# Optimization experiments

Measured on AMD Instinct MI355X. Metric: run time of the kernel, lower is better.

The kernel has to match this reference:

```python
import jax, jax.numpy as jnp
import numpy as np

NEG = 16          # negative_samples
SKIP = 1          # skip_step


def setup_inputs() -> dict:
    key = jax.random.key(0)
    k1, k2, k3, k4 = jax.random.split(key, 4)
    B, C, H, Wd = 16, 256, 32, 32
    K = 5
    maxN = (H - SKIP - 1) * Wd * B          # largest y'*x*B (k=1)
    z = jax.random.normal(k1, (B, C, H, Wd), dtype=jnp.float32)
    c = jax.random.normal(k2, (B, C, H, Wd), dtype=jnp.float32)
    # 1x1 conv weights W_k: [K, out, in]; scaled so scores are O(1)
    W = jax.random.normal(k3, (K, C, C), dtype=jnp.float32) * (1.0 / C)
    rand_index = jax.random.randint(k4, (K, maxN * NEG), 0, maxN, dtype=jnp.int32)
    return {"z": z, "c": c, "W": W, "rand_index": rand_index}


def reference(z, c, W, rand_index):
    # CLAPP/CPC hinge contrastive loss, contrast_mode='hinge', gating=None,
    # which_update='both', no_gamma=False.
    K = W.shape[0]
    total_loss = jnp.float32(0.0)
    for k in range(1, K + 1):
        # ztwk = W_k(z[:, :, k+skip:, :]) permuted to [y, x, B, C]
        zt = z[:, :, k + SKIP:, :]                              # [B, C, y, x]
        ztwk = jnp.einsum('bcyx,oc->yxbo', zt, W[k - 1])        # [y, x, B, O]
        y, x, b, o = ztwk.shape
        N = y * x * b
        # negative sampling: gather NEG random rows of flattened ztwk
        flat = ztwk.reshape(N, o)
        idx = rand_index[k - 1, :N * NEG] % N                   # in-range indices
        ztwk_shuf = flat[idx].reshape(y, x, b, NEG, o)          # [y, x, B, neg, C]
        # context = c[:, :, :-(k+skip), :] permuted to [y, x, B, C]
        ctx = jnp.transpose(c[:, :, :-(k + SKIP), :], (2, 3, 0, 1))
        scores_pos = jnp.einsum('yxbc,yxbc->yxb', ctx, ztwk)            # [y, x, B]
        scores_neg = jnp.einsum('yxbc,yxbnc->yxbn', ctx, ztwk_shuf)     # [y, x, B, neg]
        # CLAPPHingeLoss (no_gamma=False): clamped hinge terms
        losses_pos = jnp.where(scores_pos < 1.0, 1.0 - scores_pos, 0.0)
        losses_neg = jnp.where(scores_neg > -1.0, 1.0 + scores_neg, 0.0)
        # per-sample means over (neg, y, x) then mean over batch; pos is
        # replicated over neg in the original, which leaves the mean unchanged
        loss_k = losses_pos.mean(axis=(0, 1)).mean() + losses_neg.mean(axis=(0, 1, 3)).mean()
        total_loss = total_loss + loss_k
    return total_loss
```

## Files before the change

kernel.cpp:

```cpp
#include <hip/hip_runtime.h>


typedef unsigned short u16;
typedef unsigned char u8;
typedef unsigned int u32;
typedef __attribute__((ext_vector_type(8))) short bf16x8;
typedef __attribute__((ext_vector_type(4))) float f32x4;
typedef __attribute__((ext_vector_type(2))) float f32x2;

#define NEG_  16
#define MAXN_ 15360
#define TOTROWS 71680
#define NSCORE 17920
#define NPOSP  1120
#define NPARTS (NSCORE + NPOSP)

__device__ __forceinline__ u16 f2bf(float f) {
    union { u32 i; float f; } v; v.f = f;
    u32 b = v.i;
    return (u16)((b + 0x7FFFu + ((b >> 16) & 1u)) >> 16);
}

__device__ __forceinline__ size_t frag_addr(int row, int k) {
    return ((size_t)(row >> 4) * 8 + (k >> 5)) * 512
         + (size_t)((row & 15) + 16 * ((k >> 3) & 3)) * 8 + (k & 7);
}

__global__ __launch_bounds__(256) void transpose_kernel(
    const float* __restrict__ z, const float* __restrict__ cc,
    const float* __restrict__ W,
    u16* __restrict__ ztr, u8* __restrict__ ct8, u16* __restrict__ Wbf)
{
    int tid = threadIdx.x;
    if (blockIdx.z == 2) {
        if (blockIdx.y != 0 || blockIdx.x >= 320) return;
        int i4 = blockIdx.x * 256 + tid;
        float4 v = reinterpret_cast<const float4*>(W)[i4];
        int e = i4 * 4;
        int kw = e >> 16;
        int rem = e & 65535;
        int o = rem >> 8, c = rem & 255;
        size_t base = (size_t)kw * 65536 + frag_addr(o, c);
        ushort4 u;
        u.x = f2bf(v.x); u.y = f2bf(v.y); u.z = f2bf(v.z); u.w = f2bf(v.w);
        *reinterpret_cast<ushort4*>(Wbf + base) = u;
        return;
    }
    int by = blockIdx.x;
    int b = by >> 5, y = by & 31;
    int c0 = blockIdx.y * 64;
    bool is_c = (blockIdx.z == 1);
    if (is_c && y >= 30) return;
    const float* src = is_c ? cc : z;

    __shared__ float ts[64][33];
    int x = tid & 31, ci0 = tid >> 5;
#pragma unroll
    for (int i = 0; i < 8; ++i) {
        int ci = ci0 + i * 8;
        ts[ci][x] = src[(((size_t)b * 256 + c0 + ci) * 32 + y) * 32 + x];
    }
    __syncthreads();
    int cw = tid & 63, xw0 = tid >> 6;
    if (is_c) {
#pragma unroll
        for (int i = 0; i < 8; ++i) {
            int xw = xw0 + i * 4;
            float v = ts[cw][xw];
            u32 pk = __builtin_amdgcn_cvt_pk_fp8_f32(v, v, 0, false);
            ct8[(((size_t)y * 32 + xw) * 16 + b) * 256 + c0 + cw] = (u8)pk;
        }
    } else {
        int k = c0 + cw;
#pragma unroll
        for (int i = 0; i < 8; ++i) {
            int xw = xw0 + i * 4;
            int row = (y * 32 + xw) * 16 + b;
            ztr[frag_addr(row, k)] = f2bf(ts[cw][xw]);
        }
    }
}

__global__ __launch_bounds__(256) void gemm_mfma_kernel(
    const u16* __restrict__ ztr, const u16* __restrict__ Wbf,
    const u8* __restrict__ ct8,
    u8* __restrict__ ztwk8, float* __restrict__ posPart)
{
    int flat = blockIdx.x;
    int kidx, base;
    if (flat < 240)      { kidx = 0; base = 0; }
    else if (flat < 472) { kidx = 1; base = 240; }
    else if (flat < 696) { kidx = 2; base = 472; }
    else if (flat < 912) { kidx = 3; base = 696; }
    else                 { kidx = 4; base = 912; }
    int row0 = (flat - base) * 64;
    int offk = 512 * (30 * kidx - (kidx * (kidx - 1)) / 2);

    int tile0 = (((kidx + 2) * 512 + row0) >> 4);
    const u16* Bsw = Wbf + (size_t)kidx * 65536;
    u8* out = ztwk8 + ((size_t)offk + row0) * 256;

    int wid = threadIdx.x >> 6, lane = threadIdx.x & 63;
    int col0 = wid * 64;

    const u16* Abase = ztr + (size_t)tile0 * 8 * 512 + lane * 8;
    const u16* Bbase = Bsw + (size_t)wid * 4 * 8 * 512 + lane * 8;

    f32x4 acc[4][4] = {};
    bf16x8 a[4], b[4];

#pragma unroll
    for (int i = 0; i < 4; ++i)
        a[i] = *reinterpret_cast<const bf16x8*>(Abase + (size_t)i * 8 * 512);
#pragma unroll
    for (int j = 0; j < 4; ++j)
        b[j] = *reinterpret_cast<const bf16x8*>(Bbase + (size_t)j * 8 * 512);

#pragma unroll
    for (int kb = 0; kb < 8; ++kb) {
        bf16x8 a2[4], b2[4];
        if (kb < 7) {
#pragma unroll
            for (int i = 0; i < 4; ++i)
                a2[i] = *reinterpret_cast<const bf16x8*>(Abase + ((size_t)i * 8 + kb + 1) * 512);
#pragma unroll
            for (int j = 0; j < 4; ++j)
                b2[j] = *reinterpret_cast<const bf16x8*>(Bbase + ((size_t)j * 8 + kb + 1) * 512);
        }
#pragma unroll
        for (int i = 0; i < 4; ++i)
#pragma unroll
            for (int j = 0; j < 4; ++j)
                acc[i][j] = __builtin_amdgcn_mfma_f32_16x16x32_bf16(b[j], a[i], acc[i][j], 0, 0, 0);
        if (kb < 7) {
#pragma unroll
            for (int i = 0; i < 4; ++i) a[i] = a2[i];
#pragma unroll
            for (int j = 0; j < 4; ++j) b[j] = b2[j];
        }
    }

    int lr = lane & 15;
    int rq = (lane >> 4) * 4;
    __shared__ float pos[4][64];

#pragma unroll
    for (int i = 0; i < 4; ++i) {
        int local = row0 + i * 16 + lr;
        float pp = 0.f;
#pragma unroll
        for (int j = 0; j < 4; ++j) {
            u32 u = 0;
            u = __builtin_amdgcn_cvt_pk_fp8_f32(acc[i][j][0], acc[i][j][1], u, false);
            u = __builtin_amdgcn_cvt_pk_fp8_f32(acc[i][j][2], acc[i][j][3], u, true);
            *reinterpret_cast<u32*>(out + (size_t)(i * 16 + lr) * 256 + col0 + j * 16 + rq) = u;
            u32 cw_ = *reinterpret_cast<const u32*>(ct8 + (size_t)local * 256 + col0 + j * 16 + rq);
            f32x2 clo = __builtin_amdgcn_cvt_pk_f32_fp8(cw_, false);
            f32x2 chi = __builtin_amdgcn_cvt_pk_f32_fp8(cw_, true);
            pp = fmaf(acc[i][j][0], clo.x, pp);
            pp = fmaf(acc[i][j][1], clo.y, pp);
            pp = fmaf(acc[i][j][2], chi.x, pp);
            pp = fmaf(acc[i][j][3], chi.y, pp);
        }
        pp += __shfl_xor(pp, 16);
        pp += __shfl_xor(pp, 32);
        if (lane < 16) pos[wid][i * 16 + lane] = pp;
    }
    __syncthreads();

    if (threadIdx.x < 64) {
        float p = pos[0][threadIdx.x] + pos[1][threadIdx.x]
                + pos[2][threadIdx.x] + pos[3][threadIdx.x];
        float Nk = (float)((30 - kidx) * 512);
        float h = fmaxf(0.f, 1.f - p) / Nk;
#pragma unroll
        for (int s = 1; s < 64; s <<= 1) h += __shfl_xor(h, s);
        if (threadIdx.x == 0) posPart[flat] = h;
    }
}

__device__ __forceinline__ float dot16(uint4 nb, const f32x2* cp) {
    f32x2 d0 = {0.f, 0.f}, d1 = {0.f, 0.f};
    d0 += __builtin_amdgcn_cvt_pk_f32_fp8(nb.x, false) * cp[0];
    d1 += __builtin_amdgcn_cvt_pk_f32_fp8(nb.x, true)  * cp[1];
    d0 += __builtin_amdgcn_cvt_pk_f32_fp8(nb.y, false) * cp[2];
    d1 += __builtin_amdgcn_cvt_pk_f32_fp8(nb.y, true)  * cp[3];
    d0 += __builtin_amdgcn_cvt_pk_f32_fp8(nb.z, false) * cp[4];
    d1 += __builtin_amdgcn_cvt_pk_f32_fp8(nb.z, true)  * cp[5];
    d0 += __builtin_amdgcn_cvt_pk_f32_fp8(nb.w, false) * cp[6];
    d1 += __builtin_amdgcn_cvt_pk_f32_fp8(nb.w, true)  * cp[7];
    f32x2 d = d0 + d1;
    return d.x + d.y;
}

__global__ __launch_bounds__(256) void score_kernel(
    const u8* __restrict__ ztwk8, const u8* __restrict__ ct8,
    const int* __restrict__ rind, float* __restrict__ partials)
{
    __shared__ float red[4];
    int bid = blockIdx.x;
    int swb = (bid & 7) * 2240 + (bid >> 3);
    int wid = threadIdx.x >> 6, lane = threadIdx.x & 63;
    int gp = swb * 4 + wid;

    const int ends0 = 15360, ends1 = 30208, ends2 = 44544, ends3 = 58368;
    int kidx, off;
    if (gp < ends0)      { kidx = 0; off = 0; }
    else if (gp < ends1) { kidx = 1; off = ends0; }
    else if (gp < ends2) { kidx = 2; off = ends1; }
    else if (gp < ends3) { kidx = 3; off = ends2; }
    else                 { kidx = 4; off = ends3; }
    int Nk = (30 - kidx) * 512;
    int local = gp - off;

    int r = lane >> 4, c16 = lane & 15;

    const int* rbase = rind + (size_t)kidx * (MAXN_ * NEG_) + (size_t)local * NEG_ + r;
    int rv0 = rbase[0], rv1 = rbase[4], rv2 = rbase[8], rv3 = rbase[12];
    int i0 = rv0 >= Nk ? rv0 - Nk : rv0;
    int i1 = rv1 >= Nk ? rv1 - Nk : rv1;
    int i2 = rv2 >= Nk ? rv2 - Nk : rv2;
    int i3 = rv3 >= Nk ? rv3 - Nk : rv3;

    const u8* zb = ztwk8 + (size_t)off * 256 + c16 * 16;
    uint4 nb0 = *reinterpret_cast<const uint4*>(zb + (size_t)i0 * 256);
    uint4 nb1 = *reinterpret_cast<const uint4*>(zb + (size_t)i1 * 256);
    uint4 nb2 = *reinterpret_cast<const uint4*>(zb + (size_t)i2 * 256);
    uint4 nb3 = *reinterpret_cast<const uint4*>(zb + (size_t)i3 * 256);

    uint4 cw4 = *reinterpret_cast<const uint4*>(ct8 + (size_t)local * 256 + c16 * 16);
    f32x2 cp[8];
    cp[0] = __builtin_amdgcn_cvt_pk_f32_fp8(cw4.x, false);
    cp[1] = __builtin_amdgcn_cvt_pk_f32_fp8(cw4.x, true);
    cp[2] = __builtin_amdgcn_cvt_pk_f32_fp8(cw4.y, false);
    cp[3] = __builtin_amdgcn_cvt_pk_f32_fp8(cw4.y, true);
    cp[4] = __builtin_amdgcn_cvt_pk_f32_fp8(cw4.z, false);
    cp[5] = __builtin_amdgcn_cvt_pk_f32_fp8(cw4.z, true);
    cp[6] = __builtin_amdgcn_cvt_pk_f32_fp8(cw4.w, false);
    cp[7] = __builtin_amdgcn_cvt_pk_f32_fp8(cw4.w, true);

    float d0 = dot16(nb0, cp);
    float d1 = dot16(nb1, cp);
    float d2 = dot16(nb2, cp);
    float d3 = dot16(nb3, cp);

    d0 += __shfl_xor(d0, 1); d1 += __shfl_xor(d1, 1);
    d2 += __shfl_xor(d2, 1); d3 += __shfl_xor(d3, 1);
    d0 += __shfl_xor(d0, 2); d1 += __shfl_xor(d1, 2);
    d2 += __shfl_xor(d2, 2); d3 += __shfl_xor(d3, 2);
    d0 += __shfl_xor(d0, 4); d1 += __shfl_xor(d1, 4);
    d2 += __shfl_xor(d2, 4); d3 += __shfl_xor(d3, 4);
    d0 += __shfl_xor(d0, 8); d1 += __shfl_xor(d1, 8);
    d2 += __shfl_xor(d2, 8); d3 += __shfl_xor(d3, 8);

    float h = fmaxf(0.f, 1.f + d0) + fmaxf(0.f, 1.f + d1)
            + fmaxf(0.f, 1.f + d2) + fmaxf(0.f, 1.f + d3);

    float val = h * (1.0f / 16.0f);
    val += __shfl_xor(val, 16);
    val += __shfl_xor(val, 32);
    val *= 1.0f / (float)Nk;

    if (lane == 0) red[wid] = val;
    __syncthreads();
    if (threadIdx.x == 0)
        partials[bid] = red[0] + red[1] + red[2] + red[3];
}

__global__ __launch_bounds__(1024) void reduce_kernel(
    const float* __restrict__ comb, float* __restrict__ out)
{
    __shared__ float s[16];
    float a = 0.f;
    for (int i = threadIdx.x; i < NPARTS; i += 1024) a += comb[i];
#pragma unroll
    for (int t = 1; t < 64; t <<= 1) a += __shfl_xor(a, t);
    int w = threadIdx.x >> 6, lane = threadIdx.x & 63;
    if (lane == 0) s[w] = a;
    __syncthreads();
    if (threadIdx.x < 16) {
        float v = s[threadIdx.x];
#pragma unroll
        for (int t = 1; t < 16; t <<= 1) v += __shfl_xor(v, t);
        if (threadIdx.x == 0) out[0] = v;
    }
}

extern "C" void kernel_launch(void* const* d_in, const int* in_sizes, int n_in,
                              void* d_out, int out_size, void* d_ws, size_t ws_size,
                              hipStream_t stream) {
    const float* z    = (const float*)d_in[0];
    const float* c    = (const float*)d_in[1];
    const float* W    = (const float*)d_in[2];
    const int*   rind = (const int*)d_in[3];

    char* ws = (char*)d_ws;
    u16*   ztr     = (u16*)  (ws + 0);
    u8*    ct8     = (u8*)   (ws + 8388608);
    u8*    ztwk8   = (u8*)   (ws + 12320768);
    float* parts   = (float*)(ws + 30670848);
    float* posPart = (float*)(ws + 30742528);
    u16*   Wbf     = (u16*)  (ws + 30747008);
    float* out     = (float*)d_out;

    transpose_kernel<<<dim3(512, 4, 3), 256, 0, stream>>>(z, c, W, ztr, ct8, Wbf);
    gemm_mfma_kernel<<<dim3(NPOSP), 256, 0, stream>>>(ztr, Wbf, ct8, ztwk8, posPart);
    score_kernel<<<dim3(NSCORE), 256, 0, stream>>>(ztwk8, ct8, rind, parts);
    reduce_kernel<<<dim3(1), 1024, 0, stream>>>(parts, out);
}
```

Measured before the change: 72.29 us.

## Make score kernel persistent-style with ten rows per wave, simplify GEMM loads

The score kernel now launches 896 blocks of 512 threads, and each wave loops over 10 consecutive score rows, accumulating into one partial per wave. This removes the shared-memory block reduction and cuts the partial count. Random indices are now loaded as one int4 per lane instead of four strided scalar loads. The transpose also skips z rows y<2, which the GEMM never reads, and the GEMM drops its manual register double-buffering in favour of a plain per-kb load loop. The risks are lost latency hiding in the GEMM and fewer waves in flight for the gather-bound score phase.

New measurement: 75.76 us. +4.8%, slower.

```diff
diff --git a/kernel.cpp b/kernel.cpp
--- a/kernel.cpp
+++ b/kernel.cpp
@@ -11,9 +11,9 @@
 #define NEG_  16
 #define MAXN_ 15360
 #define TOTROWS 71680
-#define NSCORE 17920
+#define SWAVES 7168
 #define NPOSP  1120
-#define NPARTS (NSCORE + NPOSP)
+#define NPARTS (SWAVES + NPOSP)
 
 __device__ __forceinline__ u16 f2bf(float f) {
     union { u32 i; float f; } v; v.f = f;
@@ -50,7 +50,7 @@
     int b = by >> 5, y = by & 31;
     int c0 = blockIdx.y * 64;
     bool is_c = (blockIdx.z == 1);
-    if (is_c && y >= 30) return;
+    if (is_c ? (y >= 30) : (y < 2)) return;
     const float* src = is_c ? cc : z;
 
     __shared__ float ts[64][33];
@@ -103,41 +103,23 @@
     int wid = threadIdx.x >> 6, lane = threadIdx.x & 63;
     int col0 = wid * 64;
 
-    const u16* Abase = ztr + (size_t)tile0 * 8 * 512 + lane * 8;
-    const u16* Bbase = Bsw + (size_t)wid * 4 * 8 * 512 + lane * 8;
-
     f32x4 acc[4][4] = {};
-    bf16x8 a[4], b[4];
-
-#pragma unroll
-    for (int i = 0; i < 4; ++i)
-        a[i] = *reinterpret_cast<const bf16x8*>(Abase + (size_t)i * 8 * 512);
-#pragma unroll
-    for (int j = 0; j < 4; ++j)
-        b[j] = *reinterpret_cast<const bf16x8*>(Bbase + (size_t)j * 8 * 512);
-
-#pragma unroll
+
     for (int kb = 0; kb < 8; ++kb) {
-        bf16x8 a2[4], b2[4];
-        if (kb < 7) {
-#pragma unroll
-            for (int i = 0; i < 4; ++i)
-                a2[i] = *reinterpret_cast<const bf16x8*>(Abase + ((size_t)i * 8 + kb + 1) * 512);
-#pragma unroll
-            for (int j = 0; j < 4; ++j)
-                b2[j] = *reinterpret_cast<const bf16x8*>(Bbase + ((size_t)j * 8 + kb + 1) * 512);
-        }
+        bf16x8 a[4], b[4];
+#pragma unroll
+        for (int i = 0; i < 4; ++i)
+            a[i] = *reinterpret_cast<const bf16x8*>(
+                ztr + ((size_t)(tile0 + i) * 8 + kb) * 512 + lane * 8);
+#pragma unroll
+        for (int j = 0; j < 4; ++j)
+            b[j] = *reinterpret_cast<const bf16x8*>(
+                Bsw + ((size_t)(wid * 4 + j) * 8 + kb) * 512 + lane * 8);
 #pragma unroll
         for (int i = 0; i < 4; ++i)
 #pragma unroll
             for (int j = 0; j < 4; ++j)
                 acc[i][j] = __builtin_amdgcn_mfma_f32_16x16x32_bf16(b[j], a[i], acc[i][j], 0, 0, 0);
-        if (kb < 7) {
-#pragma unroll
-            for (int i = 0; i < 4; ++i) a[i] = a2[i];
-#pragma unroll
-            for (int j = 0; j < 4; ++j) b[j] = b2[j];
-        }
     }
 
     int lr = lane & 15;
@@ -193,78 +175,78 @@
     return d.x + d.y;
 }
 
-__global__ __launch_bounds__(256) void score_kernel(
+__global__ __launch_bounds__(512) void score_kernel(
     const u8* __restrict__ ztwk8, const u8* __restrict__ ct8,
     const int* __restrict__ rind, float* __restrict__ partials)
 {
-    __shared__ float red[4];
     int bid = blockIdx.x;
-    int swb = (bid & 7) * 2240 + (bid >> 3);
+    int swb = (bid & 7) * 112 + (bid >> 3);
     int wid = threadIdx.x >> 6, lane = threadIdx.x & 63;
-    int gp = swb * 4 + wid;
-
-    const int ends0 = 15360, ends1 = 30208, ends2 = 44544, ends3 = 58368;
-    int kidx, off;
-    if (gp < ends0)      { kidx = 0; off = 0; }
-    else if (gp < ends1) { kidx = 1; off = ends0; }
-    else if (gp < ends2) { kidx = 2; off = ends1; }
-    else if (gp < ends3) { kidx = 3; off = ends2; }
-    else                 { kidx = 4; off = ends3; }
-    int Nk = (30 - kidx) * 512;
-    int local = gp - off;
+    int g = swb * 8 + wid;
+    int base = g * 10;
 
     int r = lane >> 4, c16 = lane & 15;
-
-    const int* rbase = rind + (size_t)kidx * (MAXN_ * NEG_) + (size_t)local * NEG_ + r;
-    int rv0 = rbase[0], rv1 = rbase[4], rv2 = rbase[8], rv3 = rbase[12];
-    int i0 = rv0 >= Nk ? rv0 - Nk : rv0;
-    int i1 = rv1 >= Nk ? rv1 - Nk : rv1;
-    int i2 = rv2 >= Nk ? rv2 - Nk : rv2;
-    int i3 = rv3 >= Nk ? rv3 - Nk : rv3;
-
-    const u8* zb = ztwk8 + (size_t)off * 256 + c16 * 16;
-    uint4 nb0 = *reinterpret_cast<const uint4*>(zb + (size_t)i0 * 256);
-    uint4 nb1 = *reinterpret_cast<const uint4*>(zb + (size_t)i1 * 256);
-    uint4 nb2 = *reinterpret_cast<const uint4*>(zb + (size_t)i2 * 256);
-    uint4 nb3 = *reinterpret_cast<const uint4*>(zb + (size_t)i3 * 256);
-
-    uint4 cw4 = *reinterpret_cast<const uint4*>(ct8 + (size_t)local * 256 + c16 * 16);
-    f32x2 cp[8];
-    cp[0] = __builtin_amdgcn_cvt_pk_f32_fp8(cw4.x, false);
-    cp[1] = __builtin_amdgcn_cvt_pk_f32_fp8(cw4.x, true);
-    cp[2] = __builtin_amdgcn_cvt_pk_f32_fp8(cw4.y, false);
-    cp[3] = __builtin_amdgcn_cvt_pk_f32_fp8(cw4.y, true);
-    cp[4] = __builtin_amdgcn_cvt_pk_f32_fp8(cw4.z, false);
-    cp[5] = __builtin_amdgcn_cvt_pk_f32_fp8(cw4.z, true);
-    cp[6] = __builtin_amdgcn_cvt_pk_f32_fp8(cw4.w, false);
-    cp[7] = __builtin_amdgcn_cvt_pk_f32_fp8(cw4.w, true);
-
-    float d0 = dot16(nb0, cp);
-    float d1 = dot16(nb1, cp);
-    float d2 = dot16(nb2, cp);
-    float d3 = dot16(nb3, cp);
-
-    d0 += __shfl_xor(d0, 1); d1 += __shfl_xor(d1, 1);
-    d2 += __shfl_xor(d2, 1); d3 += __shfl_xor(d3, 1);
-    d0 += __shfl_xor(d0, 2); d1 += __shfl_xor(d1, 2);
-    d2 += __shfl_xor(d2, 2); d3 += __shfl_xor(d3, 2);
-    d0 += __shfl_xor(d0, 4); d1 += __shfl_xor(d1, 4);
-    d2 += __shfl_xor(d2, 4); d3 += __shfl_xor(d3, 4);
-    d0 += __shfl_xor(d0, 8); d1 += __shfl_xor(d1, 8);
-    d2 += __shfl_xor(d2, 8); d3 += __shfl_xor(d3, 8);
-
-    float h = fmaxf(0.f, 1.f + d0) + fmaxf(0.f, 1.f + d1)
-            + fmaxf(0.f, 1.f + d2) + fmaxf(0.f, 1.f + d3);
-
-    float val = h * (1.0f / 16.0f);
-    val += __shfl_xor(val, 16);
-    val += __shfl_xor(val, 32);
-    val *= 1.0f / (float)Nk;
-
-    if (lane == 0) red[wid] = val;
-    __syncthreads();
-    if (threadIdx.x == 0)
-        partials[bid] = red[0] + red[1] + red[2] + red[3];
+    float wsum = 0.f;
+
+#pragma unroll 2
+    for (int it = 0; it < 10; ++it) {
+        int gp = base + it;
+        int kidx, off;
+        if (gp < 15360)      { kidx = 0; off = 0; }
+        else if (gp < 30208) { kidx = 1; off = 15360; }
+        else if (gp < 44544) { kidx = 2; off = 30208; }
+        else if (gp < 58368) { kidx = 3; off = 44544; }
+        else                 { kidx = 4; off = 58368; }
+        int Nk = (30 - kidx) * 512;
+        int local = gp - off;
+
+        int4 rv = *reinterpret_cast<const int4*>(
+            rind + (size_t)kidx * (MAXN_ * NEG_) + (size_t)local * NEG_ + r * 4);
+        int i0 = rv.x >= Nk ? rv.x - Nk : rv.x;
+        int i1 = rv.y >= Nk ? rv.y - Nk : rv.y;
+        int i2 = rv.z >= Nk ? rv.z - Nk : rv.z;
+        int i3 = rv.w >= Nk ? rv.w - Nk : rv.w;
+
+        const u8* zb = ztwk8 + (size_t)off * 256 + c16 * 16;
+        uint4 nb0 = *reinterpret_cast<const uint4*>(zb + (size_t)i0 * 256);
+        uint4 nb1 = *reinterpret_cast<const uint4*>(zb + (size_t)i1 * 256);
+        uint4 nb2 = *reinterpret_cast<const uint4*>(zb + (size_t)i2 * 256);
+        uint4 nb3 = *reinterpret_cast<const uint4*>(zb + (size_t)i3 * 256);
+
+        uint4 cw4 = *reinterpret_cast<const uint4*>(ct8 + (size_t)local * 256 + c16 * 16);
+        f32x2 cp[8];
+        cp[0] = __builtin_amdgcn_cvt_pk_f32_fp8(cw4.x, false);
+        cp[1] = __builtin_amdgcn_cvt_pk_f32_fp8(cw4.x, true);
+        cp[2] = __builtin_amdgcn_cvt_pk_f32_fp8(cw4.y, false);
+        cp[3] = __builtin_amdgcn_cvt_pk_f32_fp8(cw4.y, true);
+        cp[4] = __builtin_amdgcn_cvt_pk_f32_fp8(cw4.z, false);
+        cp[5] = __builtin_amdgcn_cvt_pk_f32_fp8(cw4.z, true);
+        cp[6] = __builtin_amdgcn_cvt_pk_f32_fp8(cw4.w, false);
+        cp[7] = __builtin_amdgcn_cvt_pk_f32_fp8(cw4.w, true);
+
+        float d0 = dot16(nb0, cp);
+        float d1 = dot16(nb1, cp);
+        float d2 = dot16(nb2, cp);
+        float d3 = dot16(nb3, cp);
+
+        d0 += __shfl_xor(d0, 1); d1 += __shfl_xor(d1, 1);
+        d2 += __shfl_xor(d2, 1); d3 += __shfl_xor(d3, 1);
+        d0 += __shfl_xor(d0, 2); d1 += __shfl_xor(d1, 2);
+        d2 += __shfl_xor(d2, 2); d3 += __shfl_xor(d3, 2);
+        d0 += __shfl_xor(d0, 4); d1 += __shfl_xor(d1, 4);
+        d2 += __shfl_xor(d2, 4); d3 += __shfl_xor(d3, 4);
+        d0 += __shfl_xor(d0, 8); d1 += __shfl_xor(d1, 8);
+        d2 += __shfl_xor(d2, 8); d3 += __shfl_xor(d3, 8);
+
+        float h = fmaxf(0.f, 1.f + d0) + fmaxf(0.f, 1.f + d1)
+                + fmaxf(0.f, 1.f + d2) + fmaxf(0.f, 1.f + d3);
+        float val = h * (1.0f / 16.0f);
+        val += __shfl_xor(val, 16);
+        val += __shfl_xor(val, 32);
+        wsum += val / (float)Nk;
+    }
+
+    if (lane == 0) partials[g] = wsum;
 }
 
 __global__ __launch_bounds__(1024) void reduce_kernel(
@@ -299,12 +281,12 @@
     u8*    ct8     = (u8*)   (ws + 8388608);
     u8*    ztwk8   = (u8*)   (ws + 12320768);
     float* parts   = (float*)(ws + 30670848);
-    float* posPart = (float*)(ws + 30742528);
-    u16*   Wbf     = (u16*)  (ws + 30747008);
+    float* posPart = (float*)(ws + 30699520);
+    u16*   Wbf     = (u16*)  (ws + 30704000);
     float* out     = (float*)d_out;
 
     transpose_kernel<<<dim3(512, 4, 3), 256, 0, stream>>>(z, c, W, ztr, ct8, Wbf);
     gemm_mfma_kernel<<<dim3(NPOSP), 256, 0, stream>>>(ztr, Wbf, ct8, ztwk8, posPart);
-    score_kernel<<<dim3(NSCORE), 256, 0, stream>>>(ztwk8, ct8, rind, parts);
+    score_kernel<<<dim3(896), 512, 0, stream>>>(ztwk8, ct8, rind, parts);
     reduce_kernel<<<dim3(1), 1024, 0, stream>>>(parts, out);
 }
```
